# Performance work log

Measured on AMD Instinct MI355X. Metric: run time of the kernel, lower is better.

Reference implementation:

```python
import jax, jax.numpy as jnp
import numpy as np

B, T, H = 8, 8192, 512
E, R = 4, 16
SCALE = 0.04  # ~1/sqrt(H), keeps activations/logits in a sane range


def setup_inputs() -> dict:
    key = jax.random.key(0)
    ks = jax.random.split(key, 7)
    return {
        "x": jax.random.normal(ks[0], (B, T, H), jnp.float32),
        "gate_w": jax.random.normal(ks[1], (E, H), jnp.float32) * SCALE,
        "thr_w": jax.random.normal(ks[2], (1, H), jnp.float32) * SCALE,
        "fc1_w": jax.random.normal(ks[3], (E, H, H), jnp.float32) * SCALE,
        "lora_A": jax.random.normal(ks[4], (E, H, R), jnp.float32) * SCALE,
        "lora_B": jax.random.normal(ks[5], (E, R, H), jnp.float32) * SCALE,
        "fc2_w": jax.random.normal(ks[6], (E, H, H), jnp.float32) * SCALE,
    }


def reference(x, gate_w, thr_w, fc1_w, lora_A, lora_B, fc2_w):
    b, t, h = x.shape
    e = gate_w.shape[0]
    xf = x.reshape(-1, h)  # [N, H], N = B*T

    # Threshold-gated routing
    gate_logits = jax.nn.softmax(xf @ gate_w.T, axis=-1)          # [N, E]
    thresholds = jax.nn.sigmoid(xf @ thr_w.T) * (1.0 / e)         # [N, 1]
    adapted = gate_logits - thresholds                            # [N, E]
    selected = (adapted >= 0).astype(xf.dtype)                    # [N, E]
    weights = adapted * selected
    wsum = jnp.sum(weights, axis=-1, keepdims=True)
    wsum = jnp.where(wsum == 0, jnp.ones_like(wsum), wsum)
    weights = weights / wsum                                      # [N, E]

    # Experts: fc2(relu(fc1(x)) @ A @ B). Dense over all experts; the
    # weighted combine with zero weights matches the gather/scatter path.
    hidden = jax.nn.relu(jnp.einsum('ni,ehi->neh', xf, fc1_w))    # [N, E, H]
    lo = jnp.einsum('neh,ehr->ner', hidden, lora_A)               # [N, E, R]
    lo = jnp.einsum('ner,ero->neo', lo, lora_B)                   # [N, E, H]
    expert_out = jnp.einsum('neo,edo->ned', lo, fc2_w)            # [N, E, H]

    out = jnp.einsum('ne,ned->nd', weights, expert_out)           # [N, H]
    return out.reshape(b, t, h)
```

## Files before the change

### kernel.cpp

```cpp
#include <hip/hip_runtime.h>
#include <stdint.h>

#define NTOK 65536
#define HD   512
#define EXP  4
#define RK   16
#define BK   32

typedef __attribute__((ext_vector_type(8))) short short8;
typedef __attribute__((ext_vector_type(4))) float f32x4;

__device__ __forceinline__ unsigned short f2bf(float f) {
  union { float f; unsigned int u; } c; c.f = f;
  return (unsigned short)((c.u + 0x7fffu + ((c.u >> 16) & 1u)) >> 16);
}

__global__ void convk(const float* __restrict__ in, unsigned short* __restrict__ o, int n4) {
  int i = blockIdx.x * 256 + threadIdx.x;
  if (i < n4) {
    float4 v = ((const float4*)in)[i];
    ushort4 u;
    u.x = f2bf(v.x); u.y = f2bf(v.y); u.z = f2bf(v.z); u.w = f2bf(v.w);
    ((ushort4*)o)[i] = u;
  }
}

__global__ void prep_mt(const float* __restrict__ loraB, const float* __restrict__ fc2,
                        unsigned short* __restrict__ Mt) {
  int idx = blockIdx.x * 256 + threadIdx.x;
  int d  = idx & (HD - 1);
  int er = idx >> 9;
  int e = er >> 4, r = er & 15;
  const float4* B = (const float4*)(loraB + ((size_t)e * RK + r) * HD);
  const float4* F = (const float4*)(fc2 + ((size_t)e * HD + d) * HD);
  float a0 = 0.f, a1 = 0.f, a2 = 0.f, a3 = 0.f;
  for (int i = 0; i < HD / 4; i += 4) {
    float4 b0 = B[i],     f0 = F[i];
    float4 b1 = B[i + 1], f1 = F[i + 1];
    float4 b2 = B[i + 2], f2 = F[i + 2];
    float4 b3 = B[i + 3], f3 = F[i + 3];
    a0 += b0.x * f0.x + b0.y * f0.y + b0.z * f0.z + b0.w * f0.w;
    a1 += b1.x * f1.x + b1.y * f1.y + b1.z * f1.z + b1.w * f1.w;
    a2 += b2.x * f2.x + b2.y * f2.y + b2.z * f2.z + b2.w * f2.w;
    a3 += b3.x * f3.x + b3.y * f3.y + b3.z * f3.z + b3.w * f3.w;
  }
  Mt[d * 64 + er] = f2bf(a0 + a1 + a2 + a3);
}

__global__ void gating_k(const float* __restrict__ x, const float* __restrict__ gw,
                         const float* __restrict__ tw, float* __restrict__ gates) {
  const int lane = threadIdx.x & 63;
  const int n = blockIdx.x * 4 + (threadIdx.x >> 6);
  const float4* xr = (const float4*)(x + (size_t)n * HD);
  const float4 xa = xr[lane * 2], xb = xr[lane * 2 + 1];
  float s[5];
#pragma unroll
  for (int e = 0; e < 4; e++) {
    const float4* wr = (const float4*)(gw + e * HD);
    const float4 wa = wr[lane * 2], wb = wr[lane * 2 + 1];
    s[e] = xa.x * wa.x + xa.y * wa.y + xa.z * wa.z + xa.w * wa.w
         + xb.x * wb.x + xb.y * wb.y + xb.z * wb.z + xb.w * wb.w;
  }
  {
    const float4* wr = (const float4*)tw;
    const float4 wa = wr[lane * 2], wb = wr[lane * 2 + 1];
    s[4] = xa.x * wa.x + xa.y * wa.y + xa.z * wa.z + xa.w * wa.w
         + xb.x * wb.x + xb.y * wb.y + xb.z * wb.z + xb.w * wb.w;
  }
#pragma unroll
  for (int off = 32; off > 0; off >>= 1)
#pragma unroll
    for (int i = 0; i < 5; i++) s[i] += __shfl_xor(s[i], off, 64);
  float m = fmaxf(fmaxf(s[0], s[1]), fmaxf(s[2], s[3]));
  float e0 = expf(s[0] - m), e1 = expf(s[1] - m), e2 = expf(s[2] - m), e3 = expf(s[3] - m);
  float inv = 1.f / (e0 + e1 + e2 + e3);
  float thr = 0.25f / (1.f + expf(-s[4]));
  float a0 = e0 * inv - thr, a1 = e1 * inv - thr, a2 = e2 * inv - thr, a3 = e3 * inv - thr;
  float w0 = a0 > 0.f ? a0 : 0.f, w1 = a1 > 0.f ? a1 : 0.f;
  float w2 = a2 > 0.f ? a2 : 0.f, w3 = a3 > 0.f ? a3 : 0.f;
  float wsum = w0 + w1 + w2 + w3;
  wsum = (wsum == 0.f) ? 1.f : wsum;
  if (lane < 4) {
    float wv = lane == 0 ? w0 : lane == 1 ? w1 : lane == 2 ? w2 : w3;
    gates[(size_t)n * 4 + lane] = wv / wsum;
  }
}

__launch_bounds__(256, 2)
__global__ void fc1_lora(const unsigned short* __restrict__ xb,
                         const unsigned short* __restrict__ w1b,
                         const float* __restrict__ loraA,
                         float* __restrict__ lw) {
  __shared__ __align__(16) char smem[65536];
  const int e  = blockIdx.x;
  const int hh = blockIdx.y;
  const int n0 = blockIdx.z * 128;
  const int tid = threadIdx.x;
  const int wave = tid >> 6, lane = tid & 63, quad = lane >> 4, l16 = lane & 15;

  const unsigned short* xg = xb + (size_t)n0 * HD;
  const unsigned short* wg = w1b + (size_t)e * HD * HD + (size_t)hh * 256 * HD;

  const int srow = tid >> 2;
  const int scol = (tid & 3) << 3;

  f32x4 acc[4][8];
#pragma unroll
  for (int a = 0; a < 4; a++)
#pragma unroll
    for (int b = 0; b < 8; b++) acc[a][b] = (f32x4){0.f, 0.f, 0.f, 0.f};

  {
    short8 tx0 = *(const short8*)(xg + (size_t)srow * HD + scol);
    short8 tx1 = *(const short8*)(xg + (size_t)(srow + 64) * HD + scol);
    short8 tw0[4];
#pragma unroll
    for (int i = 0; i < 4; i++)
      tw0[i] = *(const short8*)(wg + (size_t)(srow + 64 * i) * HD + scol);
    *(short8*)(smem + (srow * BK + scol) * 2) = tx0;
    *(short8*)(smem + ((srow + 64) * BK + scol) * 2) = tx1;
#pragma unroll
    for (int i = 0; i < 4; i++)
      *(short8*)(smem + 16384 + ((srow + 64 * i) * BK + scol) * 2) = tw0[i];
  }
  __syncthreads();

  const int arow0 = (wave & 1) * 64;
  const int brow0 = (wave >> 1) * 128;

  for (int ks = 0; ks < HD / BK; ks++) {
    const int p = ks & 1;
    const bool more = (ks + 1 < HD / BK);
    short8 tx0, tx1, tw0[4];
    if (more) {
      const int k1 = (ks + 1) * BK;
      tx0 = *(const short8*)(xg + (size_t)srow * HD + k1 + scol);
      tx1 = *(const short8*)(xg + (size_t)(srow + 64) * HD + k1 + scol);
#pragma unroll
      for (int i = 0; i < 4; i++)
        tw0[i] = *(const short8*)(wg + (size_t)(srow + 64 * i) * HD + k1 + scol);
    }
    {
      const char* xs  = smem + p * 8192;
      const char* wsb = smem + 16384 + p * 16384;
      short8 af[4], bfr[8];
#pragma unroll
      for (int mf = 0; mf < 4; mf++)
        af[mf] = *(const short8*)(xs + ((arow0 + mf * 16 + l16) * BK + quad * 8) * 2);
#pragma unroll
      for (int nf = 0; nf < 8; nf++)
        bfr[nf] = *(const short8*)(wsb + ((brow0 + nf * 16 + l16) * BK + quad * 8) * 2);
#pragma unroll
      for (int mf = 0; mf < 4; mf++)
#pragma unroll
        for (int nf = 0; nf < 8; nf++)
          acc[mf][nf] = __builtin_amdgcn_mfma_f32_16x16x32_bf16(af[mf], bfr[nf], acc[mf][nf], 0, 0, 0);
    }
    if (more) {
      const int q = p ^ 1;
      *(short8*)(smem + q * 8192 + (srow * BK + scol) * 2) = tx0;
      *(short8*)(smem + q * 8192 + ((srow + 64) * BK + scol) * 2) = tx1;
#pragma unroll
      for (int i = 0; i < 4; i++)
        *(short8*)(smem + 16384 + q * 16384 + ((srow + 64 * i) * BK + scol) * 2) = tw0[i];
    }
    __syncthreads();
  }

  char* hs = smem + wave * 16384;
#pragma unroll
  for (int mf = 0; mf < 4; mf++)
#pragma unroll
    for (int nf = 0; nf < 8; nf++) {
      f32x4 v = acc[mf][nf];
      const int col = nf * 16 + l16;
#pragma unroll
      for (int i = 0; i < 4; i++) {
        float r = v[i] > 0.f ? v[i] : 0.f;
        ((unsigned short*)hs)[(mf * 16 + quad * 4 + i) * 128 + col] = f2bf(r);
      }
    }
  __syncthreads();

  const float* Ae = loraA + (size_t)e * HD * RK;
  const int hbase = hh * 256 + (wave >> 1) * 128;
  f32x4 lo[4];
#pragma unroll
  for (int mf = 0; mf < 4; mf++) lo[mf] = (f32x4){0.f, 0.f, 0.f, 0.f};
#pragma unroll
  for (int k2 = 0; k2 < 4; k2++) {
    short8 a2[4];
#pragma unroll
    for (int mf = 0; mf < 4; mf++)
      a2[mf] = *(const short8*)(hs + ((mf * 16 + l16) * 128 + k2 * 32 + quad * 8) * 2);
    union { short8 v; short s[8]; } b2;
#pragma unroll
    for (int j = 0; j < 8; j++)
      b2.s[j] = (short)f2bf(Ae[(size_t)(hbase + k2 * 32 + quad * 8 + j) * RK + l16]);
#pragma unroll
    for (int mf = 0; mf < 4; mf++)
      lo[mf] = __builtin_amdgcn_mfma_f32_16x16x32_bf16(a2[mf], b2.v, lo[mf], 0, 0, 0);
  }
  const int ntok0 = n0 + (wave & 1) * 64;
#pragma unroll
  for (int mf = 0; mf < 4; mf++)
#pragma unroll
    for (int i = 0; i < 4; i++)
      atomicAdd(lw + (size_t)(ntok0 + mf * 16 + quad * 4 + i) * 64 + e * 16 + l16, lo[mf][i]);
}

__launch_bounds__(256, 2)
__global__ void combine_k(const float* __restrict__ lw, const float* __restrict__ gates,
                          const unsigned short* __restrict__ Mt, float* __restrict__ out) {
  __shared__ __align__(16) char smem[65536];
  const int n0 = blockIdx.x * 64;
  const int tid = threadIdx.x;
  const int wave = tid >> 6, lane = tid & 63, quad = lane >> 4, l16 = lane & 15;
#pragma unroll
  for (int i = 0; i < 16; i++) {
    const int c = tid + 256 * i;
    *(uint4*)(smem + c * 16) = *(const uint4*)((const char*)Mt + c * 16);
  }
  __syncthreads();
  f32x4 acc[4][8];
#pragma unroll
  for (int a = 0; a < 4; a++)
#pragma unroll
    for (int b = 0; b < 8; b++) acc[a][b] = (f32x4){0.f, 0.f, 0.f, 0.f};
#pragma unroll
  for (int ks = 0; ks < 2; ks++) {
    short8 af[4], bfr[8];
#pragma unroll
    for (int mf = 0; mf < 4; mf++) {
      const int n = n0 + mf * 16 + l16;
      const float* lr = lw + (size_t)n * 64 + ks * 32 + quad * 8;
      float4 u0 = *(const float4*)lr;
      float4 u1 = *(const float4*)(lr + 4);
      const float g = gates[(size_t)n * 4 + ((ks * 32 + quad * 8) >> 4)];
      union { short8 v; short s[8]; } a;
      a.s[0] = (short)f2bf(u0.x * g); a.s[1] = (short)f2bf(u0.y * g);
      a.s[2] = (short)f2bf(u0.z * g); a.s[3] = (short)f2bf(u0.w * g);
      a.s[4] = (short)f2bf(u1.x * g); a.s[5] = (short)f2bf(u1.y * g);
      a.s[6] = (short)f2bf(u1.z * g); a.s[7] = (short)f2bf(u1.w * g);
      af[mf] = a.v;
    }
#pragma unroll
    for (int nf = 0; nf < 8; nf++)
      bfr[nf] = *(const short8*)(smem + ((wave * 128 + nf * 16 + l16) * 64 + ks * 32 + quad * 8) * 2);
#pragma unroll
    for (int mf = 0; mf < 4; mf++)
#pragma unroll
      for (int nf = 0; nf < 8; nf++)
        acc[mf][nf] = __builtin_amdgcn_mfma_f32_16x16x32_bf16(af[mf], bfr[nf], acc[mf][nf], 0, 0, 0);
  }
#pragma unroll
  for (int mf = 0; mf < 4; mf++)
#pragma unroll
    for (int nf = 0; nf < 8; nf++) {
      const int d = wave * 128 + nf * 16 + l16;
#pragma unroll
      for (int i = 0; i < 4; i++)
        out[(size_t)(n0 + mf * 16 + quad * 4 + i) * HD + d] = acc[mf][nf][i];
    }
}

extern "C" void kernel_launch(void* const* d_in, const int* in_sizes, int n_in,
                              void* d_out, int out_size, void* d_ws, size_t ws_size,
                              hipStream_t stream) {
  const float* x      = (const float*)d_in[0];
  const float* gate_w = (const float*)d_in[1];
  const float* thr_w  = (const float*)d_in[2];
  const float* fc1_w  = (const float*)d_in[3];
  const float* lora_A = (const float*)d_in[4];
  const float* lora_B = (const float*)d_in[5];
  const float* fc2_w  = (const float*)d_in[6];
  float* out = (float*)d_out;
  char* ws = (char*)d_ws;

  unsigned short* xb  = (unsigned short*)(ws);
  unsigned short* w1b = (unsigned short*)(ws + 67108864);
  unsigned short* Mt  = (unsigned short*)(ws + 69206016);
  float*          gts = (float*)(ws + 69271552);
  float*          lwp = (float*)(ws + 70320128);

  hipMemsetAsync(lwp, 0, (size_t)NTOK * 64 * sizeof(float), stream);
  convk<<<32768, 256, 0, stream>>>(x, xb, NTOK * HD / 4);
  convk<<<1024, 256, 0, stream>>>(fc1_w, w1b, EXP * HD * HD / 4);
  prep_mt<<<128, 256, 0, stream>>>(lora_B, fc2_w, Mt);
  gating_k<<<NTOK / 4, 256, 0, stream>>>(x, gate_w, thr_w, gts);
  fc1_lora<<<dim3(EXP, 2, NTOK / 128), 256, 0, stream>>>(xb, w1b, lora_A, lwp);
  combine_k<<<NTOK / 64, 256, 0, stream>>>(lwp, gts, Mt, out);
}
```

Baseline: 498.7 us.

## Fuse x conversion with gating; restructure fc1 GEMM with direct-to-LDS loads and 32x32 MFMA

Merges the x-to-bf16 conversion and gating into one kernel so x is read once. The fc1+LoRA kernel is rebuilt around smaller 128x128 tiles loaded with global_load_lds, XOR-swizzled LDS addressing, 32x32x16 MFMAs, a 1D grid with remapped block order for L2 reuse, and higher occupancy (3 blocks per CU, smaller LDS). The combine kernel also gets a swizzled LDS layout for the Mt matrix to reduce bank conflicts. The new GEMM drops register-staged double buffering in favour of a single LDS buffer with two barriers per K step, which may expose load latency.

Result: faster. 469.5 us (-5.8%).

```diff
diff --git a/kernel.cpp b/kernel.cpp
--- a/kernel.cpp
+++ b/kernel.cpp
@@ -7,12 +7,63 @@
 #define RK   16
 #define BK   32
 
-typedef __attribute__((ext_vector_type(8))) short short8;
-typedef __attribute__((ext_vector_type(4))) float f32x4;
+typedef __attribute__((ext_vector_type(8)))  short short8;
+typedef __attribute__((ext_vector_type(4)))  float f32x4;
+typedef __attribute__((ext_vector_type(16))) float f32x16;
 
 __device__ __forceinline__ unsigned short f2bf(float f) {
   union { float f; unsigned int u; } c; c.f = f;
   return (unsigned short)((c.u + 0x7fffu + ((c.u >> 16) & 1u)) >> 16);
+}
+
+__device__ __forceinline__ void gl_lds16(const void* g, void* l) {
+  __builtin_amdgcn_global_load_lds((const __attribute__((address_space(1))) void*)g,
+                                   (__attribute__((address_space(3))) void*)l, 16, 0, 0);
+}
+
+__global__ void convgate(const float* __restrict__ x, const float* __restrict__ gw,
+                         const float* __restrict__ tw, unsigned short* __restrict__ xbo,
+                         float* __restrict__ gates) {
+  const int lane = threadIdx.x & 63;
+  const int n = blockIdx.x * 4 + (threadIdx.x >> 6);
+  const float4* xr = (const float4*)(x + (size_t)n * HD);
+  const float4 xa = xr[lane * 2], xb = xr[lane * 2 + 1];
+  ushort4 ua, ub;
+  ua.x = f2bf(xa.x); ua.y = f2bf(xa.y); ua.z = f2bf(xa.z); ua.w = f2bf(xa.w);
+  ub.x = f2bf(xb.x); ub.y = f2bf(xb.y); ub.z = f2bf(xb.z); ub.w = f2bf(xb.w);
+  ushort4* xo = (ushort4*)(xbo + (size_t)n * HD);
+  xo[lane * 2] = ua; xo[lane * 2 + 1] = ub;
+  float s[5];
+#pragma unroll
+  for (int e = 0; e < 4; e++) {
+    const float4* wr = (const float4*)(gw + e * HD);
+    const float4 wa = wr[lane * 2], wb = wr[lane * 2 + 1];
+    s[e] = xa.x * wa.x + xa.y * wa.y + xa.z * wa.z + xa.w * wa.w
+         + xb.x * wb.x + xb.y * wb.y + xb.z * wb.z + xb.w * wb.w;
+  }
+  {
+    const float4* wr = (const float4*)tw;
+    const float4 wa = wr[lane * 2], wb = wr[lane * 2 + 1];
+    s[4] = xa.x * wa.x + xa.y * wa.y + xa.z * wa.z + xa.w * wa.w
+         + xb.x * wb.x + xb.y * wb.y + xb.z * wb.z + xb.w * wb.w;
+  }
+#pragma unroll
+  for (int off = 32; off > 0; off >>= 1)
+#pragma unroll
+    for (int i = 0; i < 5; i++) s[i] += __shfl_xor(s[i], off, 64);
+  float m = fmaxf(fmaxf(s[0], s[1]), fmaxf(s[2], s[3]));
+  float e0 = expf(s[0] - m), e1 = expf(s[1] - m), e2 = expf(s[2] - m), e3 = expf(s[3] - m);
+  float inv = 1.f / (e0 + e1 + e2 + e3);
+  float thr = 0.25f / (1.f + expf(-s[4]));
+  float a0 = e0 * inv - thr, a1 = e1 * inv - thr, a2 = e2 * inv - thr, a3 = e3 * inv - thr;
+  float w0 = a0 > 0.f ? a0 : 0.f, w1 = a1 > 0.f ? a1 : 0.f;
+  float w2 = a2 > 0.f ? a2 : 0.f, w3 = a3 > 0.f ? a3 : 0.f;
+  float wsum = w0 + w1 + w2 + w3;
+  wsum = (wsum == 0.f) ? 1.f : wsum;
+  if (lane < 4) {
+    float wv = lane == 0 ? w0 : lane == 1 ? w1 : lane == 2 ? w2 : w3;
+    gates[(size_t)n * 4 + lane] = wv / wsum;
+  }
 }
 
 __global__ void convk(const float* __restrict__ in, unsigned short* __restrict__ o, int n4) {
@@ -47,166 +98,129 @@
   Mt[d * 64 + er] = f2bf(a0 + a1 + a2 + a3);
 }
 
-__global__ void gating_k(const float* __restrict__ x, const float* __restrict__ gw,
-                         const float* __restrict__ tw, float* __restrict__ gates) {
-  const int lane = threadIdx.x & 63;
-  const int n = blockIdx.x * 4 + (threadIdx.x >> 6);
-  const float4* xr = (const float4*)(x + (size_t)n * HD);
-  const float4 xa = xr[lane * 2], xb = xr[lane * 2 + 1];
-  float s[5];
-#pragma unroll
-  for (int e = 0; e < 4; e++) {
-    const float4* wr = (const float4*)(gw + e * HD);
-    const float4 wa = wr[lane * 2], wb = wr[lane * 2 + 1];
-    s[e] = xa.x * wa.x + xa.y * wa.y + xa.z * wa.z + xa.w * wa.w
-         + xb.x * wb.x + xb.y * wb.y + xb.z * wb.z + xb.w * wb.w;
-  }
-  {
-    const float4* wr = (const float4*)tw;
-    const float4 wa = wr[lane * 2], wb = wr[lane * 2 + 1];
-    s[4] = xa.x * wa.x + xa.y * wa.y + xa.z * wa.z + xa.w * wa.w
-         + xb.x * wb.x + xb.y * wb.y + xb.z * wb.z + xb.w * wb.w;
-  }
-#pragma unroll
-  for (int off = 32; off > 0; off >>= 1)
-#pragma unroll
-    for (int i = 0; i < 5; i++) s[i] += __shfl_xor(s[i], off, 64);
-  float m = fmaxf(fmaxf(s[0], s[1]), fmaxf(s[2], s[3]));
-  float e0 = expf(s[0] - m), e1 = expf(s[1] - m), e2 = expf(s[2] - m), e3 = expf(s[3] - m);
-  float inv = 1.f / (e0 + e1 + e2 + e3);
-  float thr = 0.25f / (1.f + expf(-s[4]));
-  float a0 = e0 * inv - thr, a1 = e1 * inv - thr, a2 = e2 * inv - thr, a3 = e3 * inv - thr;
-  float w0 = a0 > 0.f ? a0 : 0.f, w1 = a1 > 0.f ? a1 : 0.f;
-  float w2 = a2 > 0.f ? a2 : 0.f, w3 = a3 > 0.f ? a3 : 0.f;
-  float wsum = w0 + w1 + w2 + w3;
-  wsum = (wsum == 0.f) ? 1.f : wsum;
-  if (lane < 4) {
-    float wv = lane == 0 ? w0 : lane == 1 ? w1 : lane == 2 ? w2 : w3;
-    gates[(size_t)n * 4 + lane] = wv / wsum;
-  }
-}
-
-__launch_bounds__(256, 2)
+__launch_bounds__(256, 3)
 __global__ void fc1_lora(const unsigned short* __restrict__ xb,
                          const unsigned short* __restrict__ w1b,
                          const float* __restrict__ loraA,
                          float* __restrict__ lw) {
-  __shared__ __align__(16) char smem[65536];
-  const int e  = blockIdx.x;
-  const int hh = blockIdx.y;
-  const int n0 = blockIdx.z * 128;
+  __shared__ __align__(16) char smem[34816];
+  const int bid = blockIdx.x;
+  const int c = bid & 7, s = bid >> 3;
+  const int eh = s & 15;
+  const int e = eh >> 2, hq = eh & 3;
+  const int ntile = ((s >> 4) << 3) | c;
+  const int n0 = ntile * 128;
   const int tid = threadIdx.x;
-  const int wave = tid >> 6, lane = tid & 63, quad = lane >> 4, l16 = lane & 15;
+  const int wave = tid >> 6, lane = tid & 63;
+  const int l16 = lane & 15, quad = lane >> 4;
+  const int l32 = lane & 31, half = lane >> 5;
 
   const unsigned short* xg = xb + (size_t)n0 * HD;
-  const unsigned short* wg = w1b + (size_t)e * HD * HD + (size_t)hh * 256 * HD;
-
-  const int srow = tid >> 2;
-  const int scol = (tid & 3) << 3;
-
-  f32x4 acc[4][8];
-#pragma unroll
-  for (int a = 0; a < 4; a++)
-#pragma unroll
-    for (int b = 0; b < 8; b++) acc[a][b] = (f32x4){0.f, 0.f, 0.f, 0.f};
-
-  {
-    short8 tx0 = *(const short8*)(xg + (size_t)srow * HD + scol);
-    short8 tx1 = *(const short8*)(xg + (size_t)(srow + 64) * HD + scol);
-    short8 tw0[4];
+  const unsigned short* wg = w1b + ((size_t)e * HD + (size_t)hq * 128) * HD;
+
+  const int slotA = tid, slotB = tid + 256;
+  const int rA = slotA >> 2, qA = (slotA & 3) ^ (rA & 3);
+  const int rB = slotB >> 2, qB = (slotB & 3) ^ (rB & 3);
+  const unsigned short* xsA = xg + (size_t)rA * HD + qA * 8;
+  const unsigned short* xsB = xg + (size_t)rB * HD + qB * 8;
+  const unsigned short* wsA = wg + (size_t)rA * HD + qA * 8;
+  const unsigned short* wsB = wg + (size_t)rB * HD + qB * 8;
+  char* ldsx = smem;
+  char* ldsw = smem + 8192;
+  char* dxA = ldsx + (wave * 64) * 16;
+  char* dxB = ldsx + (256 + wave * 64) * 16;
+  char* dwA = ldsw + (wave * 64) * 16;
+  char* dwB = ldsw + (256 + wave * 64) * 16;
+
+  const int twave = (wave & 1) * 64;
+  const int hwave = (wave >> 1) * 64;
+
+  int axo[2][2], bxo[2][2];
+#pragma unroll
+  for (int kk = 0; kk < 2; kk++)
+#pragma unroll
+    for (int b = 0; b < 2; b++) {
+      int rowa = twave + b * 32 + l32;
+      axo[kk][b] = (rowa * 4 + ((kk * 2 + half) ^ (rowa & 3))) * 16;
+      int rowb = hwave + b * 32 + l32;
+      bxo[kk][b] = (rowb * 4 + ((kk * 2 + half) ^ (rowb & 3))) * 16;
+    }
+
+  f32x16 acc[2][2];
+#pragma unroll
+  for (int mb = 0; mb < 2; mb++)
+#pragma unroll
+    for (int nb = 0; nb < 2; nb++)
+#pragma unroll
+      for (int r = 0; r < 16; r++) acc[mb][nb][r] = 0.f;
+
+  for (int ks = 0; ks < HD / BK; ks++) {
+    const int ko = ks * BK;
+    gl_lds16(xsA + ko, dxA);
+    gl_lds16(xsB + ko, dxB);
+    gl_lds16(wsA + ko, dwA);
+    gl_lds16(wsB + ko, dwB);
+    __syncthreads();
+#pragma unroll
+    for (int kk = 0; kk < 2; kk++) {
+      short8 af[2], bf[2];
+#pragma unroll
+      for (int mb = 0; mb < 2; mb++) af[mb] = *(const short8*)(ldsx + axo[kk][mb]);
+#pragma unroll
+      for (int nb = 0; nb < 2; nb++) bf[nb] = *(const short8*)(ldsw + bxo[kk][nb]);
+#pragma unroll
+      for (int mb = 0; mb < 2; mb++)
+#pragma unroll
+        for (int nb = 0; nb < 2; nb++)
+          acc[mb][nb] = __builtin_amdgcn_mfma_f32_32x32x16_bf16(af[mb], bf[nb], acc[mb][nb], 0, 0, 0);
+    }
+    __syncthreads();
+  }
+
+  unsigned short* hsm = (unsigned short*)smem;
+#pragma unroll
+  for (int mb = 0; mb < 2; mb++)
+#pragma unroll
+    for (int nb = 0; nb < 2; nb++) {
+      const int colh = hwave + nb * 32 + l32;
+#pragma unroll
+      for (int r = 0; r < 16; r++) {
+        const int tok = twave + mb * 32 + 4 * half + (r & 3) + 8 * (r >> 2);
+        float v = acc[mb][nb][r];
+        v = v > 0.f ? v : 0.f;
+        hsm[tok * 136 + colh] = f2bf(v);
+      }
+    }
+  __syncthreads();
+
+  const float* Ae = loraA + (size_t)e * HD * RK;
+  const int hA0 = hq * 128;
+  f32x4 lo[2];
+#pragma unroll
+  for (int mf = 0; mf < 2; mf++)
+#pragma unroll
+    for (int i = 0; i < 4; i++) lo[mf][i] = 0.f;
+#pragma unroll
+  for (int k2 = 0; k2 < 4; k2++) {
+    short8 a2[2];
+#pragma unroll
+    for (int mf = 0; mf < 2; mf++) {
+      const int tok = wave * 32 + mf * 16 + l16;
+      a2[mf] = *(const short8*)(hsm + tok * 136 + k2 * 32 + quad * 8);
+    }
+    union { short8 v; unsigned short s[8]; } b2;
+#pragma unroll
+    for (int j = 0; j < 8; j++)
+      b2.s[j] = f2bf(Ae[(size_t)(hA0 + k2 * 32 + quad * 8 + j) * RK + l16]);
+#pragma unroll
+    for (int mf = 0; mf < 2; mf++)
+      lo[mf] = __builtin_amdgcn_mfma_f32_16x16x32_bf16(a2[mf], b2.v, lo[mf], 0, 0, 0);
+  }
+#pragma unroll
+  for (int mf = 0; mf < 2; mf++)
 #pragma unroll
     for (int i = 0; i < 4; i++)
-      tw0[i] = *(const short8*)(wg + (size_t)(srow + 64 * i) * HD + scol);
-    *(short8*)(smem + (srow * BK + scol) * 2) = tx0;
-    *(short8*)(smem + ((srow + 64) * BK + scol) * 2) = tx1;
-#pragma unroll
-    for (int i = 0; i < 4; i++)
-      *(short8*)(smem + 16384 + ((srow + 64 * i) * BK + scol) * 2) = tw0[i];
-  }
-  __syncthreads();
-
-  const int arow0 = (wave & 1) * 64;
-  const int brow0 = (wave >> 1) * 128;
-
-  for (int ks = 0; ks < HD / BK; ks++) {
-    const int p = ks & 1;
-    const bool more = (ks + 1 < HD / BK);
-    short8 tx0, tx1, tw0[4];
-    if (more) {
-      const int k1 = (ks + 1) * BK;
-      tx0 = *(const short8*)(xg + (size_t)srow * HD + k1 + scol);
-      tx1 = *(const short8*)(xg + (size_t)(srow + 64) * HD + k1 + scol);
-#pragma unroll
-      for (int i = 0; i < 4; i++)
-        tw0[i] = *(const short8*)(wg + (size_t)(srow + 64 * i) * HD + k1 + scol);
-    }
-    {
-      const char* xs  = smem + p * 8192;
-      const char* wsb = smem + 16384 + p * 16384;
-      short8 af[4], bfr[8];
-#pragma unroll
-      for (int mf = 0; mf < 4; mf++)
-        af[mf] = *(const short8*)(xs + ((arow0 + mf * 16 + l16) * BK + quad * 8) * 2);
-#pragma unroll
-      for (int nf = 0; nf < 8; nf++)
-        bfr[nf] = *(const short8*)(wsb + ((brow0 + nf * 16 + l16) * BK + quad * 8) * 2);
-#pragma unroll
-      for (int mf = 0; mf < 4; mf++)
-#pragma unroll
-        for (int nf = 0; nf < 8; nf++)
-          acc[mf][nf] = __builtin_amdgcn_mfma_f32_16x16x32_bf16(af[mf], bfr[nf], acc[mf][nf], 0, 0, 0);
-    }
-    if (more) {
-      const int q = p ^ 1;
-      *(short8*)(smem + q * 8192 + (srow * BK + scol) * 2) = tx0;
-      *(short8*)(smem + q * 8192 + ((srow + 64) * BK + scol) * 2) = tx1;
-#pragma unroll
-      for (int i = 0; i < 4; i++)
-        *(short8*)(smem + 16384 + q * 16384 + ((srow + 64 * i) * BK + scol) * 2) = tw0[i];
-    }
-    __syncthreads();
-  }
-
-  char* hs = smem + wave * 16384;
-#pragma unroll
-  for (int mf = 0; mf < 4; mf++)
-#pragma unroll
-    for (int nf = 0; nf < 8; nf++) {
-      f32x4 v = acc[mf][nf];
-      const int col = nf * 16 + l16;
-#pragma unroll
-      for (int i = 0; i < 4; i++) {
-        float r = v[i] > 0.f ? v[i] : 0.f;
-        ((unsigned short*)hs)[(mf * 16 + quad * 4 + i) * 128 + col] = f2bf(r);
-      }
-    }
-  __syncthreads();
-
-  const float* Ae = loraA + (size_t)e * HD * RK;
-  const int hbase = hh * 256 + (wave >> 1) * 128;
-  f32x4 lo[4];
-#pragma unroll
-  for (int mf = 0; mf < 4; mf++) lo[mf] = (f32x4){0.f, 0.f, 0.f, 0.f};
-#pragma unroll
-  for (int k2 = 0; k2 < 4; k2++) {
-    short8 a2[4];
-#pragma unroll
-    for (int mf = 0; mf < 4; mf++)
-      a2[mf] = *(const short8*)(hs + ((mf * 16 + l16) * 128 + k2 * 32 + quad * 8) * 2);
-    union { short8 v; short s[8]; } b2;
-#pragma unroll
-    for (int j = 0; j < 8; j++)
-      b2.s[j] = (short)f2bf(Ae[(size_t)(hbase + k2 * 32 + quad * 8 + j) * RK + l16]);
-#pragma unroll
-    for (int mf = 0; mf < 4; mf++)
-      lo[mf] = __builtin_amdgcn_mfma_f32_16x16x32_bf16(a2[mf], b2.v, lo[mf], 0, 0, 0);
-  }
-  const int ntok0 = n0 + (wave & 1) * 64;
-#pragma unroll
-  for (int mf = 0; mf < 4; mf++)
-#pragma unroll
-    for (int i = 0; i < 4; i++)
-      atomicAdd(lw + (size_t)(ntok0 + mf * 16 + quad * 4 + i) * 64 + e * 16 + l16, lo[mf][i]);
+      atomicAdd(lw + (size_t)(n0 + wave * 32 + mf * 16 + quad * 4 + i) * 64 + e * 16 + l16, lo[mf][i]);
 }
 
 __launch_bounds__(256, 2)
@@ -218,15 +232,19 @@
   const int wave = tid >> 6, lane = tid & 63, quad = lane >> 4, l16 = lane & 15;
 #pragma unroll
   for (int i = 0; i < 16; i++) {
-    const int c = tid + 256 * i;
-    *(uint4*)(smem + c * 16) = *(const uint4*)((const char*)Mt + c * 16);
+    const int slot = tid + 256 * i;
+    const int row = slot >> 3;
+    const int g = (slot & 7) ^ (row & 7);
+    *(uint4*)(smem + slot * 16) = *(const uint4*)(Mt + row * 64 + g * 8);
   }
   __syncthreads();
   f32x4 acc[4][8];
 #pragma unroll
   for (int a = 0; a < 4; a++)
 #pragma unroll
-    for (int b = 0; b < 8; b++) acc[a][b] = (f32x4){0.f, 0.f, 0.f, 0.f};
+    for (int b = 0; b < 8; b++)
+#pragma unroll
+      for (int i = 0; i < 4; i++) acc[a][b][i] = 0.f;
 #pragma unroll
   for (int ks = 0; ks < 2; ks++) {
     short8 af[4], bfr[8];
@@ -237,16 +255,19 @@
       float4 u0 = *(const float4*)lr;
       float4 u1 = *(const float4*)(lr + 4);
       const float g = gates[(size_t)n * 4 + ((ks * 32 + quad * 8) >> 4)];
-      union { short8 v; short s[8]; } a;
-      a.s[0] = (short)f2bf(u0.x * g); a.s[1] = (short)f2bf(u0.y * g);
-      a.s[2] = (short)f2bf(u0.z * g); a.s[3] = (short)f2bf(u0.w * g);
-      a.s[4] = (short)f2bf(u1.x * g); a.s[5] = (short)f2bf(u1.y * g);
-      a.s[6] = (short)f2bf(u1.z * g); a.s[7] = (short)f2bf(u1.w * g);
+      union { short8 v; unsigned short s[8]; } a;
+      a.s[0] = f2bf(u0.x * g); a.s[1] = f2bf(u0.y * g);
+      a.s[2] = f2bf(u0.z * g); a.s[3] = f2bf(u0.w * g);
+      a.s[4] = f2bf(u1.x * g); a.s[5] = f2bf(u1.y * g);
+      a.s[6] = f2bf(u1.z * g); a.s[7] = f2bf(u1.w * g);
       af[mf] = a.v;
     }
 #pragma unroll
-    for (int nf = 0; nf < 8; nf++)
-      bfr[nf] = *(const short8*)(smem + ((wave * 128 + nf * 16 + l16) * 64 + ks * 32 + quad * 8) * 2);
+    for (int nf = 0; nf < 8; nf++) {
+      const int row = wave * 128 + nf * 16 + l16;
+      const int slot = row * 8 + ((ks * 4 + quad) ^ (row & 7));
+      bfr[nf] = *(const short8*)(smem + slot * 16);
+    }
 #pragma unroll
     for (int mf = 0; mf < 4; mf++)
 #pragma unroll
@@ -277,17 +298,16 @@
   float* out = (float*)d_out;
   char* ws = (char*)d_ws;
 
-  unsigned short* xb  = (unsigned short*)(ws);
+  unsigned short* xbp = (unsigned short*)(ws);
   unsigned short* w1b = (unsigned short*)(ws + 67108864);
   unsigned short* Mt  = (unsigned short*)(ws + 69206016);
   float*          gts = (float*)(ws + 69271552);
   float*          lwp = (float*)(ws + 70320128);
 
   hipMemsetAsync(lwp, 0, (size_t)NTOK * 64 * sizeof(float), stream);
-  convk<<<32768, 256, 0, stream>>>(x, xb, NTOK * HD / 4);
+  convgate<<<NTOK / 4, 256, 0, stream>>>(x, gate_w, thr_w, xbp, gts);
   convk<<<1024, 256, 0, stream>>>(fc1_w, w1b, EXP * HD * HD / 4);
   prep_mt<<<128, 256, 0, stream>>>(lora_B, fc2_w, Mt);
-  gating_k<<<NTOK / 4, 256, 0, stream>>>(x, gate_w, thr_w, gts);
-  fc1_lora<<<dim3(EXP, 2, NTOK / 128), 256, 0, stream>>>(xb, w1b, lora_A, lwp);
+  fc1_lora<<<8192, 256, 0, stream>>>(xbp, w1b, lora_A, lwp);
   combine_k<<<NTOK / 64, 256, 0, stream>>>(lwp, gts, Mt, out);
 }
```
